# Optimization experiments

Hardware: AMD Instinct MI355X
Metric: run time of the kernel (lower is better)

## Reference

```python
import jax, jax.numpy as jnp
import numpy as np

EPSILON = 0.1
MAX_ITER = 100
THRESHOLD = 0.001
NORMALIZE = True
INPUT_SCALE = 0.02  # keeps exp(-cost/eps) from underflowing with randn inputs


def setup_inputs() -> dict:
    key = jax.random.key(0)
    k1, k2 = jax.random.split(key)
    compressed_tokens = jax.random.normal(k1, (16, 64, 768), dtype=jnp.float32) * INPUT_SCALE
    original_tokens = jax.random.normal(k2, (16, 1024, 768), dtype=jnp.float32) * INPUT_SCALE
    return {"compressed_tokens": compressed_tokens, "original_tokens": original_tokens}


def _cost_matrix(source, target):
    # pairwise squared Euclidean distances: (n, m)
    source_sq = jnp.sum(source ** 2, axis=1, keepdims=True)          # (n, 1)
    target_sq = jnp.sum(target ** 2, axis=1, keepdims=True)          # (m, 1)
    cross = source @ target.T                                         # (n, m)
    return source_sq + target_sq.T - 2.0 * cross


def _sinkhorn(K, a, b):
    n, m = K.shape
    u0 = jnp.ones((n,), K.dtype)
    v0 = jnp.ones((m,), K.dtype)

    def step(carry, _):
        u, v, done = carry
        u_new = a / (K @ v + 1e-10)
        v_new = b / (K.T @ u_new + 1e-10)
        err = jnp.max(jnp.abs(u_new - u))
        # torch breaks AFTER the update, so the converged u,v are post-update;
        # once done, freeze u,v (equivalent to breaking out of the loop)
        u_next = jnp.where(done, u, u_new)
        v_next = jnp.where(done, v, v_new)
        done_next = done | (err < THRESHOLD)
        return (u_next, v_next, done_next), None

    (u, v, _), _ = jax.lax.scan(step, (u0, v0, jnp.asarray(False)), None, length=MAX_ITER)
    return u, v


def reference(compressed_tokens, original_tokens):
    d = compressed_tokens.shape[-1]
    src = compressed_tokens.reshape(-1, d)   # (n, d)
    tgt = original_tokens.reshape(-1, d)     # (m, d)
    n, m = src.shape[0], tgt.shape[0]

    cost = _cost_matrix(src, tgt)            # (n, m)
    K = jnp.exp(-cost / EPSILON)
    a = jnp.full((n,), 1.0 / n, dtype=cost.dtype)
    b = jnp.full((m,), 1.0 / m, dtype=cost.dtype)

    u, v = _sinkhorn(K, a, b)

    # <P, C> with P = diag(u) K diag(v)
    ot_distance = jnp.sum((u[:, None] * K * v[None, :]) * cost)
    if NORMALIZE:
        ot_distance = ot_distance / (n + m)
    ot_loss = jnp.sqrt(ot_distance + 1e-8)
    return ot_loss
```

## Files before the change

### kernel.cpp

```cpp
#include <hip/hip_runtime.h>

#define NSRC 1024
#define MTGT 16384
#define DDIM 768
#define MAXIT 100
#define NBLK 256
#define NTHR 1024
#define NGRP 16
#define GRPSZ 16

typedef __attribute__((ext_vector_type(8))) short bf16x8;
typedef __attribute__((ext_vector_type(4))) float f32x4;
typedef __attribute__((ext_vector_type(4))) unsigned short u16x4;
typedef __attribute__((ext_vector_type(8))) unsigned short u16x8;

__device__ __forceinline__ unsigned short f2bf(float f) {
  unsigned u = __float_as_uint(f);
  u += 0x7FFFu + ((u >> 16) & 1u);
  return (unsigned short)(u >> 16);
}
__device__ __forceinline__ float bf2f(unsigned short h) {
  return __uint_as_float(((unsigned)h) << 16);
}
__device__ __forceinline__ float gloadf(const float* p) {
  return __hip_atomic_load(p, __ATOMIC_RELAXED, __HIP_MEMORY_SCOPE_AGENT);
}
__device__ __forceinline__ unsigned gloadu(const unsigned* p) {
  return __hip_atomic_load(p, __ATOMIC_RELAXED, __HIP_MEMORY_SCOPE_AGENT);
}

__global__ __launch_bounds__(256) void ot_prep_kernel(
    const float* __restrict__ src, unsigned short* __restrict__ Ab,
    float* __restrict__ ssq, float* __restrict__ Kv, unsigned* __restrict__ ctrl) {
  const int gid = blockIdx.x * 256 + threadIdx.x;
  #pragma unroll
  for (int k = 0; k < 3; ++k) {
    int idx = gid + k * 65536;
    float4 a = *(const float4*)(src + (size_t)idx * 4);
    u16x4 b; b[0] = f2bf(a.x); b[1] = f2bf(a.y); b[2] = f2bf(a.z); b[3] = f2bf(a.w);
    *(u16x4*)(Ab + (size_t)idx * 4) = b;
  }
  {
    int row = gid >> 6, l = gid & 63;
    float s = 0.f;
    #pragma unroll
    for (int k = 0; k < 3; ++k) {
      float4 a = *(const float4*)(src + (size_t)row * DDIM + (l + k * 64) * 4);
      s += a.x * a.x + a.y * a.y + a.z * a.z + a.w * a.w;
    }
    #pragma unroll
    for (int off = 32; off > 0; off >>= 1) s += __shfl_down(s, off, 64);
    if (l == 0) ssq[row] = s;
  }
  for (int i = gid; i < MAXIT * NSRC; i += 65536) Kv[i] = 0.f;
  if (gid < 4096) ctrl[gid] = 0u;
}

__device__ __forceinline__ void grid_barrier(unsigned* garr, unsigned* root,
                                             unsigned* gen, unsigned& t) {
  __syncthreads();
  if (threadIdx.x == 0) {
    asm volatile("s_waitcnt vmcnt(0)" ::: "memory");
    unsigned g = (unsigned)(blockIdx.x >> 4);
    unsigned old = __hip_atomic_fetch_add(&garr[g * 64], 1u, __ATOMIC_RELAXED,
                                          __HIP_MEMORY_SCOPE_AGENT);
    if (old == t * GRPSZ + (GRPSZ - 1)) {
      unsigned r = __hip_atomic_fetch_add(root, 1u, __ATOMIC_RELAXED,
                                          __HIP_MEMORY_SCOPE_AGENT);
      if (r == t * NGRP + (NGRP - 1)) {
        __hip_atomic_store(gen, t + 1u, __ATOMIC_RELAXED, __HIP_MEMORY_SCOPE_AGENT);
      } else {
        while (gloadu(gen) < t + 1u) __builtin_amdgcn_s_sleep(1);
      }
    } else {
      while (gloadu(gen) < t + 1u) __builtin_amdgcn_s_sleep(1);
    }
    t += 1u;
  }
  __syncthreads();
}

__global__ __launch_bounds__(NTHR) void ot_fused_kernel(
    const float* __restrict__ tgt, const unsigned short* __restrict__ Ab,
    const float* __restrict__ ssq,
    float* Kv, float* ot, float* __restrict__ out,
    unsigned* garr, unsigned* root, unsigned* gen) {
  __shared__ __align__(16) unsigned short Ks[NSRC * 64];
  __shared__ __align__(16) unsigned short Bs[2][4096];
  __shared__ float ulds[NSRC];
  __shared__ float red[1104];
  __shared__ float vlds[64];
  __shared__ float tsql[64];
  __shared__ int sflag;

  const int tid = threadIdx.x, bid = blockIdx.x;
  const int w = tid >> 6, l = tid & 63;
  const int lr = l & 15, hi = l >> 4;
  const int m0 = w * 64;
  const size_t c0 = (size_t)bid * 64;
  const int rB = tid >> 4, kq = tid & 15;
  unsigned bt = 0;
  const float A_VAL = 1.0f / NSRC, B_VAL = 1.0f / MTGT;

  f32x4 acc[4][4];
  #pragma unroll
  for (int fi = 0; fi < 4; ++fi)
    #pragma unroll
    for (int fj = 0; fj < 4; ++fj) acc[fi][fj] = (f32x4){0.f, 0.f, 0.f, 0.f};

  float tsq_part = 0.f;
  {
    float4 bv = *(const float4*)(tgt + (c0 + rB) * DDIM + kq * 4);
    tsq_part += bv.x * bv.x + bv.y * bv.y + bv.z * bv.z + bv.w * bv.w;
    u16x4 bb; bb[0] = f2bf(bv.x); bb[1] = f2bf(bv.y); bb[2] = f2bf(bv.z); bb[3] = f2bf(bv.w);
    *(u16x4*)(&Bs[0][rB * 64 + (((kq >> 1) ^ (rB & 7)) << 3) + ((kq & 1) << 2)]) = bb;
  }
  __syncthreads();

  for (int kt = 0; kt < 12; ++kt) {
    float4 bv;
    if (kt < 11)
      bv = *(const float4*)(tgt + (c0 + rB) * DDIM + (kt + 1) * 64 + kq * 4);
    #pragma unroll
    for (int kc = 0; kc < 2; ++kc) {
      bf16x8 a[4];
      #pragma unroll
      for (int fi = 0; fi < 4; ++fi)
        a[fi] = *(const bf16x8*)(Ab + (size_t)(m0 + fi * 16 + lr) * DDIM +
                                 kt * 64 + kc * 32 + hi * 8);
      #pragma unroll
      for (int fj = 0; fj < 4; ++fj) {
        int rb = fj * 16 + lr;
        bf16x8 b = *(const bf16x8*)(&Bs[kt & 1][rb * 64 + ((((kc << 2) | hi) ^ (rb & 7)) << 3)]);
        #pragma unroll
        for (int fi = 0; fi < 4; ++fi)
          acc[fi][fj] = __builtin_amdgcn_mfma_f32_16x16x32_bf16(a[fi], b, acc[fi][fj], 0, 0, 0);
      }
    }
    if (kt < 11) {
      tsq_part += bv.x * bv.x + bv.y * bv.y + bv.z * bv.z + bv.w * bv.w;
      u16x4 bb; bb[0] = f2bf(bv.x); bb[1] = f2bf(bv.y); bb[2] = f2bf(bv.z); bb[3] = f2bf(bv.w);
      *(u16x4*)(&Bs[(kt + 1) & 1][rB * 64 + (((kq >> 1) ^ (rB & 7)) << 3) + ((kq & 1) << 2)]) = bb;
    }
    __syncthreads();
  }

  {
    float s = tsq_part;
    s += __shfl_xor(s, 1, 64); s += __shfl_xor(s, 2, 64);
    s += __shfl_xor(s, 4, 64); s += __shfl_xor(s, 8, 64);
    if (kq == 0) tsql[rB] = s;
  }
  __syncthreads();

  {
    const float SC = 14.426950408889634f;
    #pragma unroll
    for (int fi = 0; fi < 4; ++fi) {
      #pragma unroll
      for (int e = 0; e < 4; ++e) {
        int r = m0 + fi * 16 + hi * 4 + e;
        float sq = ssq[r];
        #pragma unroll
        for (int fj = 0; fj < 4; ++fj) {
          int c = fj * 16 + lr;
          float cost = sq + tsql[c] - 2.0f * acc[fi][fj][e];
          float k = exp2f(-SC * cost);
          Ks[r * 64 + (((c >> 3) ^ (r & 7)) << 3) + (c & 7)] = f2bf(k);
        }
      }
    }
  }
  if (tid < 64) vlds[tid] = 1.0f;
  __syncthreads();

  float uold = 1.0f;
  for (int it = 0; it < MAXIT; ++it) {
    {
      const int i = tid;
      float p = 0.f;
      #pragma unroll
      for (int lu = 0; lu < 8; ++lu) {
        int su = lu ^ (i & 7);
        u16x8 k8 = *(const u16x8*)(&Ks[i * 64 + su * 8]);
        float4 va = *(const float4*)(&vlds[lu * 8]);
        float4 vb = *(const float4*)(&vlds[lu * 8 + 4]);
        p += bf2f(k8[0]) * va.x + bf2f(k8[1]) * va.y +
             bf2f(k8[2]) * va.z + bf2f(k8[3]) * va.w +
             bf2f(k8[4]) * vb.x + bf2f(k8[5]) * vb.y +
             bf2f(k8[6]) * vb.z + bf2f(k8[7]) * vb.w;
      }
      atomicAdd(&Kv[it * NSRC + i], p);
    }
    grid_barrier(garr, root, gen, bt);
    float un, d;
    {
      float kv = gloadf(&Kv[it * NSRC + tid]);
      un = A_VAL / (kv + 1e-10f);
      d = fabsf(un - uold);
      #pragma unroll
      for (int off = 32; off > 0; off >>= 1) d = fmaxf(d, __shfl_xor(d, off, 64));
      if (l == 0) red[w] = d;
      ulds[tid] = un;
      uold = un;
    }
    __syncthreads();
    if (tid == 0) {
      float dm = red[0];
      #pragma unroll
      for (int k = 1; k < 16; ++k) dm = fmaxf(dm, red[k]);
      sflag = (dm < 0.001f) ? 1 : 0;
    }
    __syncthreads();
    const bool last = (sflag != 0) || (it == MAXIT - 1);

    {
      float* wred = (float*)Bs;
      const int c = l;
      float t = 0.f, ww = 0.f;
      #pragma unroll 8
      for (int r = 0; r < 64; ++r) {
        int i = w * 64 + r;
        float ui = ulds[i];
        float k = bf2f(Ks[i * 64 + (((c >> 3) ^ (i & 7)) << 3) + (c & 7)]);
        t += k * ui;
        if (last) ww += (k > 0.f) ? ui * k * (-0.1f * __logf(k)) : 0.f;
      }
      red[w * 68 + c] = t;
      if (last) wred[w * 68 + c] = ww;
      __syncthreads();
      if (tid < 64) {
        float tt = 0.f, wsum = 0.f;
        #pragma unroll
        for (int g = 0; g < 16; ++g) {
          tt += red[g * 68 + tid];
          if (last) wsum += wred[g * 68 + tid];
        }
        float vj = B_VAL / (tt + 1e-10f);
        vlds[tid] = vj;
        if (last) {
          float term = wsum * vj;
          #pragma unroll
          for (int off = 32; off > 0; off >>= 1) term += __shfl_down(term, off, 64);
          if (tid == 0) atomicAdd(ot, term);
        }
      }
    }
    __syncthreads();
    if (last) break;
  }

  grid_barrier(garr, root, gen, bt);
  if (bid == 0 && tid == 0)
    out[0] = sqrtf(gloadf(ot) / (float)(NSRC + MTGT) + 1e-8f);
}

extern "C" void kernel_launch(void* const* d_in, const int* in_sizes, int n_in,
                              void* d_out, int out_size, void* d_ws, size_t ws_size,
                              hipStream_t stream) {
  const float* src = (const float*)d_in[0];
  const float* tgt = (const float*)d_in[1];
  float* out = (float*)d_out;
  char* ws = (char*)d_ws;

  unsigned short* Ab = (unsigned short*)(ws);
  float* ssq = (float*)(ws + 1572864);
  float* Kv  = (float*)(ws + 1576960);
  unsigned* ctrl = (unsigned*)(ws + 1986560);
  unsigned* garr = ctrl;
  unsigned* root = ctrl + 1024;
  unsigned* gen  = ctrl + 1040;
  float* ot      = (float*)(ctrl + 1056);

  ot_prep_kernel<<<256, 256, 0, stream>>>(src, Ab, ssq, Kv, ctrl);
  ot_fused_kernel<<<NBLK, NTHR, 0, stream>>>(tgt, Ab, ssq, Kv, ot, out,
                                             garr, root, gen);
}
```

Baseline: 179.1 us.

## Replace global atomicAdd K@v reduction with partial-sum buffer and two-phase reduction

Each of the 256 blocks used to atomicAdd its 1024 partial K@v sums into a global per-iteration vector. Now each block stores its partials to a private row, and after a grid barrier each block reduces a 4-column slice across all 256 rows into a final vector. A second grid barrier follows before every block reads the result. This removes heavy atomic contention (256-way on each of 1024 addresses) and the per-iteration zeroing in the prep kernel, but adds one extra grid barrier per iteration. The same partial-buffer approach replaces the atomic on the final OT scalar.

```diff
diff --git a/kernel.cpp b/kernel.cpp
--- a/kernel.cpp
+++ b/kernel.cpp
@@ -22,6 +22,9 @@
 __device__ __forceinline__ float bf2f(unsigned short h) {
   return __uint_as_float(((unsigned)h) << 16);
 }
+__device__ __forceinline__ void gstoref(float* p, float x) {
+  __hip_atomic_store(p, x, __ATOMIC_RELAXED, __HIP_MEMORY_SCOPE_AGENT);
+}
 __device__ __forceinline__ float gloadf(const float* p) {
   return __hip_atomic_load(p, __ATOMIC_RELAXED, __HIP_MEMORY_SCOPE_AGENT);
 }
@@ -31,7 +34,7 @@
 
 __global__ __launch_bounds__(256) void ot_prep_kernel(
     const float* __restrict__ src, unsigned short* __restrict__ Ab,
-    float* __restrict__ ssq, float* __restrict__ Kv, unsigned* __restrict__ ctrl) {
+    float* __restrict__ ssq, unsigned* __restrict__ ctrl) {
   const int gid = blockIdx.x * 256 + threadIdx.x;
   #pragma unroll
   for (int k = 0; k < 3; ++k) {
@@ -52,7 +55,6 @@
     for (int off = 32; off > 0; off >>= 1) s += __shfl_down(s, off, 64);
     if (l == 0) ssq[row] = s;
   }
-  for (int i = gid; i < MAXIT * NSRC; i += 65536) Kv[i] = 0.f;
   if (gid < 4096) ctrl[gid] = 0u;
 }
 
@@ -83,7 +85,7 @@
 __global__ __launch_bounds__(NTHR) void ot_fused_kernel(
     const float* __restrict__ tgt, const unsigned short* __restrict__ Ab,
     const float* __restrict__ ssq,
-    float* Kv, float* ot, float* __restrict__ out,
+    float* Kvp, float* Kvf, float* otp, float* __restrict__ out,
     unsigned* garr, unsigned* root, unsigned* gen) {
   __shared__ __align__(16) unsigned short Ks[NSRC * 64];
   __shared__ __align__(16) unsigned short Bs[2][4096];
@@ -190,14 +192,27 @@
              bf2f(k8[4]) * vb.x + bf2f(k8[5]) * vb.y +
              bf2f(k8[6]) * vb.z + bf2f(k8[7]) * vb.w;
       }
-      atomicAdd(&Kv[it * NSRC + i], p);
+      gstoref(&Kvp[(size_t)bid * NSRC + tid], p);
     }
     grid_barrier(garr, root, gen, bt);
-    float un, d;
     {
-      float kv = gloadf(&Kv[it * NSRC + tid]);
-      un = A_VAL / (kv + 1e-10f);
-      d = fabsf(un - uold);
+      float s = gloadf(&Kvp[(size_t)(tid >> 2) * NSRC + (bid << 2) + (tid & 3)]);
+      s += __shfl_xor(s, 4, 64);  s += __shfl_xor(s, 8, 64);
+      s += __shfl_xor(s, 16, 64); s += __shfl_xor(s, 32, 64);
+      if (l < 4) red[w * 4 + l] = s;
+      __syncthreads();
+      if (tid < 4) {
+        float t = 0.f;
+        #pragma unroll
+        for (int g = 0; g < 16; ++g) t += red[g * 4 + tid];
+        gstoref(&Kvf[(bid << 2) + tid], t);
+      }
+    }
+    grid_barrier(garr, root, gen, bt);
+    {
+      float kv = gloadf(&Kvf[tid]);
+      float un = A_VAL / (kv + 1e-10f);
+      float d = fabsf(un - uold);
       #pragma unroll
       for (int off = 32; off > 0; off >>= 1) d = fmaxf(d, __shfl_xor(d, off, 64));
       if (l == 0) red[w] = d;
@@ -242,7 +257,7 @@
           float term = wsum * vj;
           #pragma unroll
           for (int off = 32; off > 0; off >>= 1) term += __shfl_down(term, off, 64);
-          if (tid == 0) atomicAdd(ot, term);
+          if (tid == 0) gstoref(&otp[bid], term);
         }
       }
     }
@@ -251,8 +266,19 @@
   }
 
   grid_barrier(garr, root, gen, bt);
-  if (bid == 0 && tid == 0)
-    out[0] = sqrtf(gloadf(ot) / (float)(NSRC + MTGT) + 1e-8f);
+  if (bid == 0) {
+    float s = (tid < NBLK) ? gloadf(&otp[tid]) : 0.f;
+    if (tid < NBLK) {
+      #pragma unroll
+      for (int off = 32; off > 0; off >>= 1) s += __shfl_down(s, off, 64);
+      if (l == 0) red[w] = s;
+    }
+    __syncthreads();
+    if (tid == 0) {
+      float tot = red[0] + red[1] + red[2] + red[3];
+      out[0] = sqrtf(tot / (float)(NSRC + MTGT) + 1e-8f);
+    }
+  }
 }
 
 extern "C" void kernel_launch(void* const* d_in, const int* in_sizes, int n_in,
@@ -265,14 +291,15 @@
 
   unsigned short* Ab = (unsigned short*)(ws);
   float* ssq = (float*)(ws + 1572864);
-  float* Kv  = (float*)(ws + 1576960);
-  unsigned* ctrl = (unsigned*)(ws + 1986560);
+  float* Kvp = (float*)(ws + 1576960);
+  float* Kvf = (float*)(ws + 2625536);
+  float* otp = (float*)(ws + 2629632);
+  unsigned* ctrl = (unsigned*)(ws + 2630656);
   unsigned* garr = ctrl;
   unsigned* root = ctrl + 1024;
   unsigned* gen  = ctrl + 1040;
-  float* ot      = (float*)(ctrl + 1056);
-
-  ot_prep_kernel<<<256, 256, 0, stream>>>(src, Ab, ssq, Kv, ctrl);
-  ot_fused_kernel<<<NBLK, NTHR, 0, stream>>>(tgt, Ab, ssq, Kv, ot, out,
+
+  ot_prep_kernel<<<256, 256, 0, stream>>>(src, Ab, ssq, ctrl);
+  ot_fused_kernel<<<NBLK, NTHR, 0, stream>>>(tgt, Ab, ssq, Kvp, Kvf, otp, out,
                                              garr, root, gen);
 }
```

Result: no change. 178.5 us (-0.3%).
